# Kernel tuning notes

Measured on AMD Instinct MI355X. Metric: run time of the kernel, lower is better.

## Reference

```python
import jax, jax.numpy as jnp
import numpy as np

N_NODES = 100000


def setup_inputs() -> dict:
    key = jax.random.key(0)
    k1, k2, k3 = jax.random.split(key, 3)
    x = jax.random.normal(k1, (N_NODES, 128), dtype=jnp.float32)
    edge_index = jax.random.randint(k2, (2, 1600000), 0, N_NODES, dtype=jnp.int64)
    # TAGConv K=1 linear weight: maps concat([x, Ax]) (2*in) -> out; stored as [(K+1)*in, out]
    W = (jax.random.normal(k3, (256, 128), dtype=jnp.float32) / np.sqrt(256.0)).astype(jnp.float32)
    return {"x": x, "edge_index": edge_index, "W": W}


def reference(x, edge_index, W):
    src, dst = edge_index[0], edge_index[1]
    n = x.shape[0]
    ones = jnp.ones(src.shape[0], dtype=x.dtype)
    # gcn_norm without self-loops: degree from edge weights scattered at target
    deg = jax.ops.segment_sum(ones, dst, num_segments=n)
    dis = jnp.where(deg > 0, jax.lax.rsqrt(jnp.where(deg > 0, deg, 1.0)), 0.0)
    norm = dis[src] * dis[dst]  # [E]
    # message passing: out[dst] += norm * x[src]
    msgs = x[src] * norm[:, None]  # [E, in]
    agg = jax.ops.segment_sum(msgs, dst, num_segments=n)  # [N, in]
    h = jnp.concatenate([x, agg], axis=1)  # [N, 2*in]
    return h @ W  # [N, out]
```

## Files before the change

kernel.cpp:

```cpp
#include <hip/hip_runtime.h>


#define GCN_F 128
#define BINCAP 9216
#define NBIN_USED 196
#define EPACK_ROWS 14112

typedef __attribute__((ext_vector_type(8))) short frag_ab;
typedef __attribute__((ext_vector_type(4))) float frag_cd;

__device__ __forceinline__ unsigned short f2bf(float f) {
    unsigned int u = __float_as_uint(f);
    unsigned int r = (u + 0x7FFFu + ((u >> 16) & 1u)) >> 16;
    return (unsigned short)r;
}

__device__ __forceinline__ int detect_is32(const unsigned int* ei32, int* s_is32) {
    if (threadIdx.x == 0) *s_is32 = 0;
    __syncthreads();
    unsigned int v = 0;
    for (int i = threadIdx.x; i < 2048; i += blockDim.x) v |= ei32[2 * i + 1];
    if (v != 0u) atomicOr(s_is32, 1);
    __syncthreads();
    return *s_is32;
}

__device__ __forceinline__ int load_idx(const int* ei, int is32, long long pos) {
    if (is32) return ei[pos];
    return ((const int2*)ei)[pos].x;
}

__global__ __launch_bounds__(256) void bscatter_kernel(const int* __restrict__ ei,
                                                       int* __restrict__ gcur,
                                                       unsigned int* __restrict__ epack,
                                                       int E, int EB,
                                                       const float* __restrict__ W,
                                                       unsigned short* __restrict__ wt) {
    if ((int)blockIdx.x >= EB) {
        int c = blockIdx.x - EB;
        int k = threadIdx.x;
        wt[c * 256 + k] = f2bf(W[k * GCN_F + c]);
        return;
    }
    __shared__ int h[4][256];
    __shared__ int lcur[256];
    __shared__ int s_is32;
    int tid = threadIdx.x;
    int wv = tid >> 6;
    for (int i = tid; i < 1024; i += 256) ((int*)h)[i] = 0;
    int is32 = detect_is32((const unsigned int*)ei, &s_is32);
    int base = blockIdx.x * 4096;
    unsigned int pk[16];
    int bn[16];
#pragma unroll
    for (int j = 0; j < 16; ++j) {
        int e = base + j * 256 + tid;
        bn[j] = -1;
        pk[j] = 0;
        if (e < E) {
            int src = load_idx(ei, is32, e);
            int dst = load_idx(ei, is32, (long long)E + e);
            pk[j] = (unsigned int)src | (((unsigned int)dst & 511u) << 17);
            bn[j] = dst >> 9;
            atomicAdd(&h[wv][bn[j]], 1);
        }
    }
    __syncthreads();
    {
        int cnt = h[0][tid] + h[1][tid] + h[2][tid] + h[3][tid];
        if (cnt > 0) {
            int run = atomicAdd(&gcur[tid], cnt);
            if (run + cnt > BINCAP) run = BINCAP - cnt;
            lcur[tid] = tid * BINCAP + run;
        }
    }
    __syncthreads();
#pragma unroll
    for (int j = 0; j < 16; ++j) {
        if (bn[j] >= 0) {
            int pos = atomicAdd(&lcur[bn[j]], 1);
            epack[pos] = pk[j];
        }
    }
}

__global__ __launch_bounds__(256) void cscan_kernel(const int* __restrict__ gcur,
                                                    int* __restrict__ cs) {
    __shared__ int tmp[256];
    int tid = threadIdx.x;
    int v = min(gcur[tid], BINCAP);
    tmp[tid] = v;
    __syncthreads();
    for (int off = 1; off < 256; off <<= 1) {
        int t = (tid >= off) ? tmp[tid - off] : 0;
        __syncthreads();
        tmp[tid] += t;
        __syncthreads();
    }
    cs[tid] = tmp[tid] - v;
    if (tid == 255) cs[256] = tmp[255];
}

__global__ __launch_bounds__(512) void fcsr_kernel(const unsigned int* __restrict__ epack,
                                                   const int* __restrict__ gcur,
                                                   const int* __restrict__ cs,
                                                   int* __restrict__ start,
                                                   float* __restrict__ dis,
                                                   int* __restrict__ ebuf,
                                                   const float4* __restrict__ x4,
                                                   unsigned short* __restrict__ hbuf,
                                                   int N, int E, int CB) {
    int tid = threadIdx.x;
    if ((int)blockIdx.x >= CB) {
        int chunk = blockIdx.x - CB;
        int g = EPACK_ROWS * 32 + chunk * 512 + tid;
        if (g < N * 32) {
            int r = g >> 5, q = g & 31;
            float4 v = x4[(long long)r * 32 + q];
            ushort4 o;
            o.x = f2bf(v.x); o.y = f2bf(v.y); o.z = f2bf(v.z); o.w = f2bf(v.w);
            *(ushort4*)((char*)hbuf + ((unsigned)r << 9) + q * 8) = o;
        }
        return;
    }
    __shared__ int lh[512];
    __shared__ int sc[512];
    int c = blockIdx.x;
    lh[tid] = 0;
    __syncthreads();
    int b = c * BINCAP;
    int e = b + min(gcur[c], BINCAP);
    for (int i = b + tid; i < e; i += 512) {
        atomicAdd(&lh[(epack[i] >> 17) & 511u], 1);
    }
    __syncthreads();
    sc[tid] = lh[tid];
    __syncthreads();
    for (int off = 1; off < 512; off <<= 1) {
        int t = (tid >= off) ? sc[tid - off] : 0;
        __syncthreads();
        sc[tid] += t;
        __syncthreads();
    }
    int d = lh[tid];
    int gs = cs[c] + sc[tid] - d;
    int node = c * 512 + tid;
    if (node < N) {
        start[node] = gs;
        dis[node] = (d > 0) ? rsqrtf((float)d) : 0.0f;
    }
    __syncthreads();
    sc[tid] = gs;
    if (c == 0 && tid == 0) start[N] = E;
    __syncthreads();
    for (int i = b + tid; i < e; i += 512) {
        unsigned int v = epack[i];
        int pos = atomicAdd(&sc[(v >> 17) & 511u], 1);
        ebuf[pos] = (int)(v & 0x1FFFFu);
    }
}

__global__ __launch_bounds__(256) void xbf_lo_kernel(const float4* __restrict__ x4,
                                                     unsigned short* __restrict__ hbuf) {
    int g = blockIdx.x * 256 + threadIdx.x;
    if (g >= EPACK_ROWS * 32) return;
    int r = g >> 5, q = g & 31;
    float4 v = x4[(long long)r * 32 + q];
    ushort4 o;
    o.x = f2bf(v.x); o.y = f2bf(v.y); o.z = f2bf(v.z); o.w = f2bf(v.w);
    *(ushort4*)((char*)hbuf + ((unsigned)r << 9) + q * 8) = o;
}

__global__ __launch_bounds__(256) void gather_kernel(unsigned short* __restrict__ hbuf,
                                                     const int* __restrict__ ebuf,
                                                     const int* __restrict__ start,
                                                     const float* __restrict__ dis,
                                                     int N) {
    int node = blockIdx.x * 4 + (threadIdx.x >> 6);
    if (node >= N) return;
    int lane = threadIdx.x & 63;
    int slot = lane >> 4;
    unsigned int subb = (lane & 15) * 16;
    int s = start[node];
    int d = start[node + 1] - s;
    float nd = dis[node];
    const char* hc = (const char*)hbuf;
    float acc[8];
#pragma unroll
    for (int i = 0; i < 8; ++i) acc[i] = 0.0f;

    for (int base = 0; base < d; base += 64) {
        int cn = min(64, d - base);
        int eid = 0; float dv = 0.0f;
        if (lane < cn) {
            eid = ebuf[s + base + lane];
            dv = dis[eid];
        }
        int njj = (cn + 3) >> 2;
#pragma unroll 4
        for (int j = 0; j < njj; ++j) {
            int tt = 4 * j + slot;
            int src = __shfl(eid, tt);
            float f = __shfl(dv, tt);
            uint4 u = *(const uint4*)(hc + (((unsigned)src << 9) + subb));
            acc[0] += f * __uint_as_float(u.x << 16);
            acc[1] += f * __uint_as_float(u.x);
            acc[2] += f * __uint_as_float(u.y << 16);
            acc[3] += f * __uint_as_float(u.y);
            acc[4] += f * __uint_as_float(u.z << 16);
            acc[5] += f * __uint_as_float(u.z);
            acc[6] += f * __uint_as_float(u.w << 16);
            acc[7] += f * __uint_as_float(u.w);
        }
    }
#pragma unroll
    for (int i = 0; i < 8; ++i) {
        acc[i] += __shfl_xor(acc[i], 16);
        acc[i] += __shfl_xor(acc[i], 32);
    }
    if (slot == 0) {
        uint4 o;
        o.x = (unsigned int)f2bf(acc[0] * nd) | ((unsigned int)f2bf(acc[1] * nd) << 16);
        o.y = (unsigned int)f2bf(acc[2] * nd) | ((unsigned int)f2bf(acc[3] * nd) << 16);
        o.z = (unsigned int)f2bf(acc[4] * nd) | ((unsigned int)f2bf(acc[5] * nd) << 16);
        o.w = (unsigned int)f2bf(acc[6] * nd) | ((unsigned int)f2bf(acc[7] * nd) << 16);
        *(uint4*)((char*)hbuf + (((unsigned)node << 9) + 256 + subb)) = o;
    }
}

#define GEMM_BM 128
__global__ __launch_bounds__(256) void gemm_mfma_kernel(
        const unsigned short* h,
        const unsigned short* __restrict__ wt,
        float* out, int N) {
    int wave = threadIdx.x >> 6;
    int lane = threadIdx.x & 63;
    int lr = lane & 15;
    int kh = lane >> 4;
    int rowbase = blockIdx.x * GEMM_BM + wave * 32;
    const char* hc = (const char*)h;

    frag_cd acc[2][8];
#pragma unroll
    for (int rt = 0; rt < 2; ++rt)
#pragma unroll
        for (int ct = 0; ct < 8; ++ct) acc[rt][ct] = (frag_cd)0.0f;

    for (int ks = 0; ks < 8; ++ks) {
        frag_ab a[2];
#pragma unroll
        for (int rt = 0; rt < 2; ++rt) {
            int r = rowbase + rt * 16 + lr;
            r = min(r, N - 1);
            a[rt] = *(const frag_ab*)(hc + (((unsigned)r << 9) + (unsigned)(ks * 64 + kh * 16)));
        }
#pragma unroll
        for (int ct = 0; ct < 8; ++ct) {
            int c = ct * 16 + lr;
            frag_ab b = *(const frag_ab*)(wt + c * 256 + ks * 32 + kh * 8);
#pragma unroll
            for (int rt = 0; rt < 2; ++rt) {
                acc[rt][ct] = __builtin_amdgcn_mfma_f32_16x16x32_bf16(a[rt], b, acc[rt][ct], 0, 0, 0);
            }
        }
    }
#pragma unroll
    for (int rt = 0; rt < 2; ++rt) {
#pragma unroll
        for (int ct = 0; ct < 8; ++ct) {
#pragma unroll
            for (int reg = 0; reg < 4; ++reg) {
                int r = rowbase + rt * 16 + kh * 4 + reg;
                if (r < N) out[r * GCN_F + ct * 16 + lr] = acc[rt][ct][reg];
            }
        }
    }
}

extern "C" void kernel_launch(void* const* d_in, const int* in_sizes, int n_in,
                              void* d_out, int out_size, void* d_ws, size_t ws_size,
                              hipStream_t stream) {
    const float* x  = (const float*)d_in[0];
    const int*   ei = (const int*)d_in[1];
    const float* W  = (const float*)d_in[2];
    float* out = (float*)d_out;

    const int N = in_sizes[0] / GCN_F;
    const int E = in_sizes[1] / 2;

    char* ws = (char*)d_ws;
    int*   gcur  = (int*)ws;
    int*   cs    = (int*)(ws + 1024);
    float* dis   = (float*)(ws + 8192);
    int*   start = (int*)(ws + 408192);
    int*   ebuf  = (int*)(ws + 808208);
    unsigned short* wt = (unsigned short*)(ws + 7208208);

    unsigned int*   epack = (unsigned int*)d_out;
    unsigned short* h     = (unsigned short*)d_out;

    const int CB = (N + 511) / 512;
    const int EB = (E + 4095) / 4096;
    const int XBHI = ((N - EPACK_ROWS) * 32 + 511) / 512;
    const int XBLO = (EPACK_ROWS * 32 + 255) / 256;

    hipMemsetAsync(d_ws, 0, 1024, stream);

    bscatter_kernel<<<EB + 128, 256, 0, stream>>>(ei, gcur, epack, E, EB, W, wt);
    cscan_kernel<<<1, 256, 0, stream>>>(gcur, cs);
    fcsr_kernel<<<CB + XBHI, 512, 0, stream>>>(epack, gcur, cs, start, dis, ebuf,
                                               (const float4*)x, h, N, E, CB);
    xbf_lo_kernel<<<XBLO, 256, 0, stream>>>((const float4*)x, h);
    gather_kernel<<<(N + 3) / 4, 256, 0, stream>>>(h, ebuf, start, dis, N);
    gemm_mfma_kernel<<<(N + GEMM_BM - 1) / GEMM_BM, 256, 0, stream>>>(h, wt, out, N);
}
```

Before: 164.8 us.

## Fold column scan into fcsr and move bf16 x conversion into workspace

Removes the single-block cscan kernel by having every fcsr block redo the 256-bin prefix scan in shared memory. When the workspace is large enough, x is converted to a compact bf16 buffer in the workspace, with a 256-byte row stride, during the bscatter launch. This drops the separate low-rows conversion kernel and shrinks the gather's row footprint. Gather and GEMM now read x and the aggregate from separate buffers. The cost is redundant scan work in every fcsr block and extra conversion blocks in bscatter.

```diff
diff --git a/kernel.cpp b/kernel.cpp
--- a/kernel.cpp
+++ b/kernel.cpp
@@ -3,7 +3,6 @@
 
 #define GCN_F 128
 #define BINCAP 9216
-#define NBIN_USED 196
 #define EPACK_ROWS 14112
 
 typedef __attribute__((ext_vector_type(8))) short frag_ab;
@@ -28,6 +27,14 @@
 __device__ __forceinline__ int load_idx(const int* ei, int is32, long long pos) {
     if (is32) return ei[pos];
     return ((const int2*)ei)[pos].x;
+}
+
+__device__ __forceinline__ void xbf_store(const float4* x4, char* xb, int xs, int g) {
+    int r = g >> 5, q = g & 31;
+    float4 v = x4[(long long)r * 32 + q];
+    ushort4 o;
+    o.x = f2bf(v.x); o.y = f2bf(v.y); o.z = f2bf(v.z); o.w = f2bf(v.w);
+    *(ushort4*)(xb + ((unsigned)r << xs) + q * 8) = o;
 }
 
 __global__ __launch_bounds__(256) void bscatter_kernel(const int* __restrict__ ei,
@@ -35,17 +42,24 @@
                                                        unsigned int* __restrict__ epack,
                                                        int E, int EB,
                                                        const float* __restrict__ W,
-                                                       unsigned short* __restrict__ wt) {
+                                                       unsigned short* __restrict__ wt,
+                                                       const float4* __restrict__ x4,
+                                                       char* __restrict__ xb,
+                                                       int xs, int g0, int Ntot) {
+    int tid = threadIdx.x;
+    if ((int)blockIdx.x >= EB + 128) {
+        int g = g0 + (blockIdx.x - (EB + 128)) * 256 + tid;
+        if (g < Ntot * 32) xbf_store(x4, xb, xs, g);
+        return;
+    }
     if ((int)blockIdx.x >= EB) {
         int c = blockIdx.x - EB;
-        int k = threadIdx.x;
-        wt[c * 256 + k] = f2bf(W[k * GCN_F + c]);
+        wt[c * 256 + tid] = f2bf(W[tid * GCN_F + c]);
         return;
     }
     __shared__ int h[4][256];
     __shared__ int lcur[256];
     __shared__ int s_is32;
-    int tid = threadIdx.x;
     int wv = tid >> 6;
     for (int i = tid; i < 1024; i += 256) ((int*)h)[i] = 0;
     int is32 = detect_is32((const unsigned int*)ei, &s_is32);
@@ -84,49 +98,33 @@
     }
 }
 
-__global__ __launch_bounds__(256) void cscan_kernel(const int* __restrict__ gcur,
-                                                    int* __restrict__ cs) {
-    __shared__ int tmp[256];
-    int tid = threadIdx.x;
-    int v = min(gcur[tid], BINCAP);
-    tmp[tid] = v;
-    __syncthreads();
-    for (int off = 1; off < 256; off <<= 1) {
-        int t = (tid >= off) ? tmp[tid - off] : 0;
-        __syncthreads();
-        tmp[tid] += t;
-        __syncthreads();
-    }
-    cs[tid] = tmp[tid] - v;
-    if (tid == 255) cs[256] = tmp[255];
-}
-
 __global__ __launch_bounds__(512) void fcsr_kernel(const unsigned int* __restrict__ epack,
                                                    const int* __restrict__ gcur,
-                                                   const int* __restrict__ cs,
                                                    int* __restrict__ start,
                                                    float* __restrict__ dis,
                                                    int* __restrict__ ebuf,
-                                                   const float4* __restrict__ x4,
-                                                   unsigned short* __restrict__ hbuf,
-                                                   int N, int E, int CB) {
-    int tid = threadIdx.x;
-    if ((int)blockIdx.x >= CB) {
-        int chunk = blockIdx.x - CB;
-        int g = EPACK_ROWS * 32 + chunk * 512 + tid;
-        if (g < N * 32) {
-            int r = g >> 5, q = g & 31;
-            float4 v = x4[(long long)r * 32 + q];
-            ushort4 o;
-            o.x = f2bf(v.x); o.y = f2bf(v.y); o.z = f2bf(v.z); o.w = f2bf(v.w);
-            *(ushort4*)((char*)hbuf + ((unsigned)r << 9) + q * 8) = o;
-        }
-        return;
-    }
+                                                   int N) {
+    __shared__ int stmp[256];
+    __shared__ int s_base, s_total;
     __shared__ int lh[512];
     __shared__ int sc[512];
     int c = blockIdx.x;
+    int tid = threadIdx.x;
+    int v0 = 0;
+    if (tid < 256) {
+        v0 = min(gcur[tid], BINCAP);
+        stmp[tid] = v0;
+    }
     lh[tid] = 0;
+    __syncthreads();
+    for (int off = 1; off < 256; off <<= 1) {
+        int t = (tid < 256 && tid >= off) ? stmp[tid - off] : 0;
+        __syncthreads();
+        if (tid < 256) stmp[tid] += t;
+        __syncthreads();
+    }
+    if (tid == c) s_base = stmp[tid] - v0;
+    if (tid == 255) s_total = stmp[255];
     __syncthreads();
     int b = c * BINCAP;
     int e = b + min(gcur[c], BINCAP);
@@ -143,7 +141,7 @@
         __syncthreads();
     }
     int d = lh[tid];
-    int gs = cs[c] + sc[tid] - d;
+    int gs = s_base + sc[tid] - d;
     int node = c * 512 + tid;
     if (node < N) {
         start[node] = gs;
@@ -151,7 +149,7 @@
     }
     __syncthreads();
     sc[tid] = gs;
-    if (c == 0 && tid == 0) start[N] = E;
+    if (c == 0 && tid == 0) start[N] = s_total;
     __syncthreads();
     for (int i = b + tid; i < e; i += 512) {
         unsigned int v = epack[i];
@@ -161,17 +159,14 @@
 }
 
 __global__ __launch_bounds__(256) void xbf_lo_kernel(const float4* __restrict__ x4,
-                                                     unsigned short* __restrict__ hbuf) {
+                                                     char* __restrict__ xb, int xs) {
     int g = blockIdx.x * 256 + threadIdx.x;
     if (g >= EPACK_ROWS * 32) return;
-    int r = g >> 5, q = g & 31;
-    float4 v = x4[(long long)r * 32 + q];
-    ushort4 o;
-    o.x = f2bf(v.x); o.y = f2bf(v.y); o.z = f2bf(v.z); o.w = f2bf(v.w);
-    *(ushort4*)((char*)hbuf + ((unsigned)r << 9) + q * 8) = o;
-}
-
-__global__ __launch_bounds__(256) void gather_kernel(unsigned short* __restrict__ hbuf,
+    xbf_store(x4, xb, xs, g);
+}
+
+__global__ __launch_bounds__(256) void gather_kernel(const char* __restrict__ xb, int xs,
+                                                     char* __restrict__ aggb,
                                                      const int* __restrict__ ebuf,
                                                      const int* __restrict__ start,
                                                      const float* __restrict__ dis,
@@ -184,7 +179,6 @@
     int s = start[node];
     int d = start[node + 1] - s;
     float nd = dis[node];
-    const char* hc = (const char*)hbuf;
     float acc[8];
 #pragma unroll
     for (int i = 0; i < 8; ++i) acc[i] = 0.0f;
@@ -202,7 +196,7 @@
             int tt = 4 * j + slot;
             int src = __shfl(eid, tt);
             float f = __shfl(dv, tt);
-            uint4 u = *(const uint4*)(hc + (((unsigned)src << 9) + subb));
+            uint4 u = *(const uint4*)(xb + (((unsigned)src << xs) + subb));
             acc[0] += f * __uint_as_float(u.x << 16);
             acc[1] += f * __uint_as_float(u.x);
             acc[2] += f * __uint_as_float(u.y << 16);
@@ -224,13 +218,14 @@
         o.y = (unsigned int)f2bf(acc[2] * nd) | ((unsigned int)f2bf(acc[3] * nd) << 16);
         o.z = (unsigned int)f2bf(acc[4] * nd) | ((unsigned int)f2bf(acc[5] * nd) << 16);
         o.w = (unsigned int)f2bf(acc[6] * nd) | ((unsigned int)f2bf(acc[7] * nd) << 16);
-        *(uint4*)((char*)hbuf + (((unsigned)node << 9) + 256 + subb)) = o;
+        *(uint4*)(aggb + (((unsigned)node << 9) + 256 + subb)) = o;
     }
 }
 
 #define GEMM_BM 128
 __global__ __launch_bounds__(256) void gemm_mfma_kernel(
-        const unsigned short* h,
+        const char* __restrict__ xb, int xs,
+        const char* aggb,
         const unsigned short* __restrict__ wt,
         float* out, int N) {
     int wave = threadIdx.x >> 6;
@@ -238,7 +233,6 @@
     int lr = lane & 15;
     int kh = lane >> 4;
     int rowbase = blockIdx.x * GEMM_BM + wave * 32;
-    const char* hc = (const char*)h;
 
     frag_cd acc[2][8];
 #pragma unroll
@@ -246,13 +240,17 @@
 #pragma unroll
         for (int ct = 0; ct < 8; ++ct) acc[rt][ct] = (frag_cd)0.0f;
 
+#pragma unroll
     for (int ks = 0; ks < 8; ++ks) {
         frag_ab a[2];
 #pragma unroll
         for (int rt = 0; rt < 2; ++rt) {
             int r = rowbase + rt * 16 + lr;
             r = min(r, N - 1);
-            a[rt] = *(const frag_ab*)(hc + (((unsigned)r << 9) + (unsigned)(ks * 64 + kh * 16)));
+            const char* ap = (ks < 4)
+                ? (xb   + (((unsigned)r << xs) + (unsigned)(ks * 64 + kh * 16)))
+                : (aggb + (((unsigned)r << 9) + (unsigned)(256 + (ks - 4) * 64 + kh * 16)));
+            a[rt] = *(const frag_ab*)ap;
         }
 #pragma unroll
         for (int ct = 0; ct < 8; ++ct) {
@@ -290,27 +288,36 @@
 
     char* ws = (char*)d_ws;
     int*   gcur  = (int*)ws;
-    int*   cs    = (int*)(ws + 1024);
     float* dis   = (float*)(ws + 8192);
     int*   start = (int*)(ws + 408192);
     int*   ebuf  = (int*)(ws + 808208);
     unsigned short* wt = (unsigned short*)(ws + 7208208);
-
-    unsigned int*   epack = (unsigned int*)d_out;
-    unsigned short* h     = (unsigned short*)d_out;
+    char*  xb_ws = ws + 7274496;
+
+    unsigned int* epack = (unsigned int*)d_out;
+    char*         aggb  = (char*)d_out;
+
+    const size_t WS_NEED = 7274496 + (size_t)N * 256;
+    const bool bigws = ws_size >= WS_NEED;
+
+    char* xb = bigws ? xb_ws : (char*)d_out;
+    int   xs = bigws ? 8 : 9;
+    int g0 = bigws ? 0 : EPACK_ROWS * 32;
+    int XR = (N * 32 - g0 + 255) / 256;
 
     const int CB = (N + 511) / 512;
     const int EB = (E + 4095) / 4096;
-    const int XBHI = ((N - EPACK_ROWS) * 32 + 511) / 512;
-    const int XBLO = (EPACK_ROWS * 32 + 255) / 256;
 
     hipMemsetAsync(d_ws, 0, 1024, stream);
 
-    bscatter_kernel<<<EB + 128, 256, 0, stream>>>(ei, gcur, epack, E, EB, W, wt);
-    cscan_kernel<<<1, 256, 0, stream>>>(gcur, cs);
-    fcsr_kernel<<<CB + XBHI, 512, 0, stream>>>(epack, gcur, cs, start, dis, ebuf,
-                                               (const float4*)x, h, N, E, CB);
-    xbf_lo_kernel<<<XBLO, 256, 0, stream>>>((const float4*)x, h);
-    gather_kernel<<<(N + 3) / 4, 256, 0, stream>>>(h, ebuf, start, dis, N);
-    gemm_mfma_kernel<<<(N + GEMM_BM - 1) / GEMM_BM, 256, 0, stream>>>(h, wt, out, N);
-}
+    bscatter_kernel<<<EB + 128 + XR, 256, 0, stream>>>(
+        ei, gcur, epack, E, EB, W, wt, (const float4*)x, xb, xs, g0, N);
+    fcsr_kernel<<<CB, 512, 0, stream>>>(epack, gcur, start, dis, ebuf, N);
+    if (!bigws) {
+        xbf_lo_kernel<<<(EPACK_ROWS * 32 + 255) / 256, 256, 0, stream>>>(
+            (const float4*)x, xb, xs);
+    }
+    gather_kernel<<<(N + 3) / 4, 256, 0, stream>>>(xb, xs, aggb, ebuf, start, dis, N);
+    gemm_mfma_kernel<<<(N + GEMM_BM - 1) / GEMM_BM, 256, 0, stream>>>(
+        xb, xs, aggb, wt, out, N);
+}
```

New measurement: 160.8 us. 2.4% less time.
